# Optimization experiments

Measured on AMD Instinct MI355X. Metric: run time of the kernel, lower is better.

## Reference

```python
import jax, jax.numpy as jnp
import numpy as np

N, IN_DIM, OUT_DIM, E = 50000, 64, 64, 800000


def setup_inputs() -> dict:
    key = jax.random.key(0)
    k1, k2, k3, k4 = jax.random.split(key, 4)
    x = jax.random.normal(k1, (N, IN_DIM), dtype=jnp.float32)
    edge_index = jax.random.randint(k2, (2, E), 0, N, dtype=jnp.int64)
    # nn.Linear(in_dim, out_dim): weight [out, in], bias [out]
    bound = 1.0 / np.sqrt(IN_DIM)
    W = jax.random.uniform(k3, (OUT_DIM, IN_DIM), minval=-bound, maxval=bound, dtype=jnp.float32)
    b = jax.random.uniform(k4, (OUT_DIM,), minval=-bound, maxval=bound, dtype=jnp.float32)
    return {"x": x, "edge_index": edge_index, "W": W, "b": b}


def reference(x, edge_index, W, b):
    row, col = edge_index[0], edge_index[1]
    n = x.shape[0]
    # deg = bincount(row, minlength=N) + 1e-6, shape [N, 1]
    deg = jnp.zeros((n,), dtype=jnp.float32).at[row].add(1.0)[:, None] + 1e-6
    # agg[row] += x[col]  (gather + scatter-add)
    agg = jnp.zeros_like(x).at[row].add(x[col])
    agg = agg / deg
    return agg @ W.T + b
```

## Files before the change

kernel.cpp:

```cpp
#include <hip/hip_runtime.h>
#include <hip/hip_bf16.h>

#define N_NODES 50000
#define DIM 64
#define N_EDGES 800000
#define CAP 64
#define NTHR 256
#define GB_ROWS 32
#define SLICE 6250
#define NGROUP 196
#define TOTAL_BLOCKS (NGROUP * 24)
#define CHUNK_EDGES 2048


static __device__ inline unsigned int f2bf(float f) {
    __hip_bfloat16 h = __float2bfloat16(f);
    return (unsigned int)*reinterpret_cast<unsigned short*>(&h);
}
static __device__ inline float bf_lo(unsigned int u) { return __uint_as_float(u << 16); }
static __device__ inline float bf_hi(unsigned int u) { return __uint_as_float(u & 0xffff0000u); }

__global__ __launch_bounds__(NTHR, 8) void place_gemm_kernel(
    const int* __restrict__ ei, const float* __restrict__ x,
    const float* __restrict__ W, int* __restrict__ count,
    int* csr, unsigned short* __restrict__ yb)
{
    __shared__ uint4  Wb[512];
    __shared__ float4 xs4[GB_ROWS * 16];

    int t = threadIdx.x;
    int b = blockIdx.x;
    int m = b % 24;

    if (m < 8) {
        int g  = (b / 24) * 8 + m;
        int R0 = g * GB_ROWS;
        const float4* x4 = (const float4*)x;
        for (int i = t; i < GB_ROWS * 16; i += NTHR) {
            int q = R0 * 16 + i;
            xs4[i] = (q < N_NODES * 16) ? x4[q] : make_float4(0.f, 0.f, 0.f, 0.f);
        }
        for (int k = t; k < 512; k += NTHR) {
            int o = k & 63, j8 = k >> 6;
            const float* wr = W + o * DIM + j8 * 8;
            uint4 uw;
            uw.x = f2bf(wr[0]) | (f2bf(wr[1]) << 16);
            uw.y = f2bf(wr[2]) | (f2bf(wr[3]) << 16);
            uw.z = f2bf(wr[4]) | (f2bf(wr[5]) << 16);
            uw.w = f2bf(wr[6]) | (f2bf(wr[7]) << 16);
            Wb[k] = uw;
        }
        __syncthreads();

        int w = t >> 6, l = t & 63;
#pragma unroll
        for (int i = 0; i < 8; i++) {
            int rl = w * 8 + i;
            int r  = R0 + rl;
            if (r < N_NODES) {
                float acc = 0.f;
#pragma unroll
                for (int j8 = 0; j8 < 8; j8++) {
                    uint4  wq = Wb[j8 * 64 + l];
                    float4 x0 = xs4[rl * 16 + 2 * j8];
                    float4 x1 = xs4[rl * 16 + 2 * j8 + 1];
                    acc += x0.x * bf_lo(wq.x) + x0.y * bf_hi(wq.x)
                         + x0.z * bf_lo(wq.y) + x0.w * bf_hi(wq.y)
                         + x1.x * bf_lo(wq.z) + x1.y * bf_hi(wq.z)
                         + x1.z * bf_lo(wq.w) + x1.w * bf_hi(wq.w);
                }
                yb[(size_t)r * DIM + l] = (unsigned short)f2bf(acc);
            }
        }
    } else {
        int s    = b & 7;
        int lo   = s * SLICE;
        int q    = (b / 24) * 2 + ((m - 8) >> 3);
        int e0   = q * CHUNK_EDGES + t * 8;
        if (e0 < N_EDGES) {
            const int4* rp = (const int4*)(ei + e0);
            int4 ra = rp[0];
            int4 rb = rp[1];
            int rows[8] = {ra.x, ra.y, ra.z, ra.w, rb.x, rb.y, rb.z, rb.w};
#pragma unroll
            for (int k = 0; k < 8; k++) {
                if ((unsigned)(rows[k] - lo) < (unsigned)SLICE) {
                    int col = ei[N_EDGES + e0 + k];
                    int pos = atomicAdd(&count[rows[k]], 1);
                    if (pos < CAP) csr[rows[k] * CAP + pos] = col;
                }
            }
        }
    }
}

__global__ __launch_bounds__(NTHR) void agg_kernel(
    const unsigned short* __restrict__ yb, const int* __restrict__ count,
    const int* csr, const float* __restrict__ bias, float* out)
{
    int t   = threadIdx.x;
    int w   = t >> 6;
    int l   = t & 63;
    int sub = l & 7;
    int grp = l >> 3;
    int sb  = blockIdx.x & 7;
    int i   = blockIdx.x >> 3;
    int rl  = i * 4 + w;
    if (rl >= SLICE) return;
    int r = sb * SLICE + rl;

    int deg = count[r];
    int dc  = deg < CAP ? deg : CAP;
    int myc = csr[(size_t)r * CAP + l];

    const uint4* ybq = (const uint4*)yb;
    float s[8];
#pragma unroll
    for (int q = 0; q < 8; q++) s[q] = 0.f;

    bool valid = grp < dc;
    {
        int c0 = __shfl(myc, grp);
        int cs = valid ? c0 : 0;
        uint4 v = ybq[(size_t)cs * 8 + sub];
        for (int jb = 8; jb < dc; jb += 8) {
            int  j2     = jb + grp;
            int  c2     = __shfl(myc, j2);
            bool valid2 = j2 < dc;
            int  cs2    = valid2 ? c2 : 0;
            uint4 v2 = ybq[(size_t)cs2 * 8 + sub];
            if (valid) {
                s[0] += bf_lo(v.x); s[1] += bf_hi(v.x);
                s[2] += bf_lo(v.y); s[3] += bf_hi(v.y);
                s[4] += bf_lo(v.z); s[5] += bf_hi(v.z);
                s[6] += bf_lo(v.w); s[7] += bf_hi(v.w);
            }
            v = v2; valid = valid2;
        }
        if (valid) {
            s[0] += bf_lo(v.x); s[1] += bf_hi(v.x);
            s[2] += bf_lo(v.y); s[3] += bf_hi(v.y);
            s[4] += bf_lo(v.z); s[5] += bf_hi(v.z);
            s[6] += bf_lo(v.w); s[7] += bf_hi(v.w);
        }
    }
#pragma unroll
    for (int q = 0; q < 8; q++) {
        s[q] += __shfl_xor(s[q], 8);
        s[q] += __shfl_xor(s[q], 16);
        s[q] += __shfl_xor(s[q], 32);
    }

    if (grp == 0) {
        float inv_d = 1.0f / ((float)deg + 1e-6f);
        float4 b0 = ((const float4*)bias)[2 * sub];
        float4 b1 = ((const float4*)bias)[2 * sub + 1];
        float4 o0 = make_float4(s[0] * inv_d + b0.x, s[1] * inv_d + b0.y,
                                s[2] * inv_d + b0.z, s[3] * inv_d + b0.w);
        float4 o1 = make_float4(s[4] * inv_d + b1.x, s[5] * inv_d + b1.y,
                                s[6] * inv_d + b1.z, s[7] * inv_d + b1.w);
        ((float4*)(out + (size_t)r * DIM))[2 * sub]     = o0;
        ((float4*)(out + (size_t)r * DIM))[2 * sub + 1] = o1;
    }
}

extern "C" void kernel_launch(void* const* d_in, const int* in_sizes, int n_in,
                              void* d_out, int out_size, void* d_ws, size_t ws_size,
                              hipStream_t stream) {
    const float* x    = (const float*)d_in[0];
    const int*   ei   = (const int*)d_in[1];
    const float* W    = (const float*)d_in[2];
    const float* bias = (const float*)d_in[3];
    float* out = (float*)d_out;

    int*            count = (int*)d_ws;
    unsigned short* yb    = (unsigned short*)((char*)d_ws + 262144);
    int*            csr   = (int*)d_out;

    hipMemsetAsync(count, 0, N_NODES * sizeof(int), stream);
    place_gemm_kernel<<<TOTAL_BLOCKS, NTHR, 0, stream>>>(ei, x, W, count, csr, yb);
    agg_kernel<<<8 * 1563, NTHR, 0, stream>>>(yb, count, csr, bias, out);
}
```

Baseline: 129.8 us.

## Compute x@W^T tile with bf16 MFMA using split hi/lo inputs and swizzled LDS

Replaces the scalar per-lane dot-product GEMM in the placement kernel with MFMA 16x16x32 bf16 instructions. x is split into bf16 hi and lo parts to keep accuracy. Shared-memory layouts for x and W are XOR-swizzled to avoid bank conflicts. An early exit skips blocks past the row range. The GEMM blocks share the launch with edge-placement blocks, so the gain may be hidden by the atomic scatter work.

```diff
diff --git a/kernel.cpp b/kernel.cpp
--- a/kernel.cpp
+++ b/kernel.cpp
@@ -13,6 +13,9 @@
 #define CHUNK_EDGES 2048
 
 
+typedef __attribute__((ext_vector_type(8))) short bf16x8;
+typedef __attribute__((ext_vector_type(4))) float f32x4;
+
 static __device__ inline unsigned int f2bf(float f) {
     __hip_bfloat16 h = __float2bfloat16(f);
     return (unsigned int)*reinterpret_cast<unsigned short*>(&h);
@@ -25,8 +28,8 @@
     const float* __restrict__ W, int* __restrict__ count,
     int* csr, unsigned short* __restrict__ yb)
 {
+    __shared__ float4 xs4[GB_ROWS * 16];
     __shared__ uint4  Wb[512];
-    __shared__ float4 xs4[GB_ROWS * 16];
 
     int t = threadIdx.x;
     int b = blockIdx.x;
@@ -35,41 +38,73 @@
     if (m < 8) {
         int g  = (b / 24) * 8 + m;
         int R0 = g * GB_ROWS;
-        const float4* x4 = (const float4*)x;
-        for (int i = t; i < GB_ROWS * 16; i += NTHR) {
-            int q = R0 * 16 + i;
-            xs4[i] = (q < N_NODES * 16) ? x4[q] : make_float4(0.f, 0.f, 0.f, 0.f);
-        }
-        for (int k = t; k < 512; k += NTHR) {
-            int o = k & 63, j8 = k >> 6;
-            const float* wr = W + o * DIM + j8 * 8;
-            uint4 uw;
-            uw.x = f2bf(wr[0]) | (f2bf(wr[1]) << 16);
-            uw.y = f2bf(wr[2]) | (f2bf(wr[3]) << 16);
-            uw.z = f2bf(wr[4]) | (f2bf(wr[5]) << 16);
-            uw.w = f2bf(wr[6]) | (f2bf(wr[7]) << 16);
-            Wb[k] = uw;
-        }
-        __syncthreads();
-
-        int w = t >> 6, l = t & 63;
-#pragma unroll
-        for (int i = 0; i < 8; i++) {
-            int rl = w * 8 + i;
-            int r  = R0 + rl;
-            if (r < N_NODES) {
-                float acc = 0.f;
-#pragma unroll
-                for (int j8 = 0; j8 < 8; j8++) {
-                    uint4  wq = Wb[j8 * 64 + l];
-                    float4 x0 = xs4[rl * 16 + 2 * j8];
-                    float4 x1 = xs4[rl * 16 + 2 * j8 + 1];
-                    acc += x0.x * bf_lo(wq.x) + x0.y * bf_hi(wq.x)
-                         + x0.z * bf_lo(wq.y) + x0.w * bf_hi(wq.y)
-                         + x1.x * bf_lo(wq.z) + x1.y * bf_hi(wq.z)
-                         + x1.z * bf_lo(wq.w) + x1.w * bf_hi(wq.w);
-                }
-                yb[(size_t)r * DIM + l] = (unsigned short)f2bf(acc);
+        if (R0 < N_NODES) {
+            const float4* x4 = (const float4*)x;
+            for (int i = t; i < GB_ROWS * 16; i += NTHR) {
+                int r = i >> 4, c = i & 15;
+                int q = (R0 + r) * 16 + c;
+                float4 v = (q < N_NODES * 16) ? x4[q]
+                                              : make_float4(0.f, 0.f, 0.f, 0.f);
+                xs4[(r << 4) | (c ^ (r & 15))] = v;
+            }
+            for (int i = t; i < 512; i += NTHR) {
+                int n = i >> 3, kg = i & 7;
+                const float* wr = W + n * DIM + kg * 8;
+                uint4 uw;
+                uw.x = f2bf(wr[0]) | (f2bf(wr[1]) << 16);
+                uw.y = f2bf(wr[2]) | (f2bf(wr[3]) << 16);
+                uw.z = f2bf(wr[4]) | (f2bf(wr[5]) << 16);
+                uw.w = f2bf(wr[6]) | (f2bf(wr[7]) << 16);
+                Wb[(n << 3) | (kg ^ (n & 7))] = uw;
+            }
+            __syncthreads();
+
+            int w  = t >> 6, l = t & 63;
+            int rt = w >> 1, ch = w & 1;
+            int lm = l & 15, lg = l >> 4;
+            int mloc = rt * 16 + lm;
+
+            f32x4 acc0 = {0.f, 0.f, 0.f, 0.f};
+            f32x4 acc1 = {0.f, 0.f, 0.f, 0.f};
+#pragma unroll
+            for (int kc = 0; kc < 2; kc++) {
+                int c0 = kc * 8 + lg * 2;
+                float4 xa = xs4[(mloc << 4) | ((c0    ) ^ lm)];
+                float4 xb = xs4[(mloc << 4) | ((c0 + 1) ^ lm)];
+                float xv[8] = {xa.x, xa.y, xa.z, xa.w, xb.x, xb.y, xb.z, xb.w};
+                bf16x8 ahi, alo;
+#pragma unroll
+                for (int j = 0; j < 8; j++) {
+                    unsigned hb = f2bf(xv[j]);
+                    float lo = xv[j] - __uint_as_float(hb << 16);
+                    ahi[j] = (short)hb;
+                    alo[j] = (short)f2bf(lo);
+                }
+                int kgg = kc * 4 + lg;
+#pragma unroll
+                for (int ctl = 0; ctl < 2; ctl++) {
+                    int n = (ch * 2 + ctl) * 16 + lm;
+                    uint4 wq = Wb[(n << 3) | (kgg ^ (n & 7))];
+                    bf16x8 bfr = *reinterpret_cast<bf16x8*>(&wq);
+                    if (ctl == 0) {
+                        acc0 = __builtin_amdgcn_mfma_f32_16x16x32_bf16(ahi, bfr, acc0, 0, 0, 0);
+                        acc0 = __builtin_amdgcn_mfma_f32_16x16x32_bf16(alo, bfr, acc0, 0, 0, 0);
+                    } else {
+                        acc1 = __builtin_amdgcn_mfma_f32_16x16x32_bf16(ahi, bfr, acc1, 0, 0, 0);
+                        acc1 = __builtin_amdgcn_mfma_f32_16x16x32_bf16(alo, bfr, acc1, 0, 0, 0);
+                    }
+                }
+            }
+#pragma unroll
+            for (int ctl = 0; ctl < 2; ctl++) {
+                f32x4 acc = ctl ? acc1 : acc0;
+                int n = (ch * 2 + ctl) * 16 + lm;
+#pragma unroll
+                for (int q = 0; q < 4; q++) {
+                    int rr = R0 + rt * 16 + lg * 4 + q;
+                    if (rr < N_NODES)
+                        yb[(size_t)rr * DIM + n] = (unsigned short)f2bf(acc[q]);
+                }
             }
         }
     } else {
```

Result: no change. 128.7 us (-0.9%).
